# Kernel tuning notes

Measured on AMD Instinct MI355X. Metric: run time of the kernel, lower is better.

The kernel has to match this reference:

```python
import jax, jax.numpy as jnp
import numpy as np

TEMPERATURE = 1.0  # SpriteAssembler.compositing_temperature
EPS = 1e-6


def setup_inputs() -> dict:
    key = jax.random.key(0)
    k1, k2 = jax.random.split(key)
    B, H, W, N = 8, 256, 256, 64
    shapes = jax.random.uniform(k1, (B, H, W, N), dtype=jnp.float32)  # occupancy in [0,1]
    depths = jax.random.normal(k2, (B, N), dtype=jnp.float32)
    return {"shapes": shapes, "depths": depths}


def reference(shapes, depths):
    # custom_composite: depth-ordered log-space alpha compositing.
    # mask_i = s_i * prod_j (1 - s_j) ** tanh(relu((d_j - d_i)/T)), then normalize.
    d = depths / max(TEMPERATURE, 1e-6)                      # [B, N]
    s = jnp.clip(shapes, EPS, 1.0 - EPS)                     # [B, H, W, N]
    # occlusion weights: w[b, i, j] = tanh(relu(d_j - d_i))
    w = jnp.tanh(jax.nn.relu(d[:, None, :] - d[:, :, None]))  # [B, N, N]
    log1m = jnp.log1p(-s)                                    # log(1 - s), [B, H, W, N]
    # log_mask_i = log(s_i) + sum_j log(1 - s_j) * w[i, j]  (j == i term is 0 since w[i,i]=0)
    log_masks = jnp.log(s) + jnp.einsum('bhwj,bij->bhwi', log1m, w)
    unnormalized = jnp.exp(log_masks)                        # [B, H, W, N]
    masks = unnormalized / (jnp.sum(unnormalized, axis=-1, keepdims=True) + EPS)
    return masks
```

## Files before the change

kernel.cpp:

```cpp
#include <hip/hip_runtime.h>


typedef __attribute__((ext_vector_type(8))) _Float16 half8;
typedef __attribute__((ext_vector_type(4))) float floatx4;

#define EPSF 1e-6f

__device__ inline float fast_exp2(float x){ return __builtin_amdgcn_exp2f(x); }
__device__ inline float fast_log2(float x){ return __builtin_amdgcn_logf(x); }
__device__ inline float fast_rcp (float x){ return __builtin_amdgcn_rcpf(x); }

__global__ __launch_bounds__(256, 2) void sprite_mfma_kernel(
    const float* __restrict__ shapes,
    const float* __restrict__ depths,
    float* __restrict__ out)
{
    const int wave  = threadIdx.x >> 6;
    const int lane  = threadIdx.x & 63;
    const int batch = blockIdx.x >> 7;
    const int rblk  = blockIdx.x & 127;
    const int wid   = rblk * 4 + wave;

    __shared__ float dsh[64];
    if (threadIdx.x < 64) dsh[threadIdx.x] = depths[batch * 64 + threadIdx.x];
    __syncthreads();

    const int c = lane & 15;
    const int q = lane >> 4;

    half8 Aw[4][2];
    #pragma unroll
    for (int it = 0; it < 4; ++it) {
        float di = dsh[it * 16 + c];
        #pragma unroll
        for (int kt = 0; kt < 2; ++kt) {
            half8 h;
            #pragma unroll
            for (int jj = 0; jj < 8; ++jj) {
                int j = kt * 32 + q * 8 + jj;
                float x = fmaxf(dsh[j] - di, 0.0f);
                float e = fast_exp2(x * 2.885390082f);
                h[jj] = (_Float16)((e - 1.0f) * fast_rcp(e + 1.0f));
            }
            Aw[it][kt] = h;
        }
    }

    half8 idlo, idhi;
    #pragma unroll
    for (int jj = 0; jj < 8; ++jj) {
        idlo[jj] = (q * 8 + jj == c)      ? (_Float16)1.0f : (_Float16)0.0f;
        idhi[jj] = (q * 8 + jj == 16 + c) ? (_Float16)1.0f : (_Float16)0.0f;
    }

    const long pxbase = (long)batch * 65536 + (long)wid * 128;
    const float* sp = shapes + (pxbase + c) * 64;
    float* op = out + (pxbase + c) * 64;

    float4 pf0 = *(const float4*)(sp + q * 8);
    float4 pf1 = *(const float4*)(sp + q * 8 + 4);
    float4 pf2 = *(const float4*)(sp + q * 8 + 32);
    float4 pf3 = *(const float4*)(sp + q * 8 + 36);

    for (int tile = 0; tile < 8; ++tile) {
        float4 s0 = pf0, s1 = pf1, s2 = pf2, s3 = pf3;
        if (tile < 7) {
            const float* sn = sp + (tile + 1) * 16 * 64 + q * 8;
            pf0 = *(const float4*)(sn);
            pf1 = *(const float4*)(sn + 4);
            pf2 = *(const float4*)(sn + 32);
            pf3 = *(const float4*)(sn + 36);
        }

        float sv[16] = {s0.x, s0.y, s0.z, s0.w, s1.x, s1.y, s1.z, s1.w,
                        s2.x, s2.y, s2.z, s2.w, s3.x, s3.y, s3.z, s3.w};
        half8 B_lo, B_hi;
        half8 C_lo, C_hi;
        #pragma unroll
        for (int e = 0; e < 8; ++e) {
            float slo = fminf(fmaxf(sv[e],     EPSF), 1.0f - EPSF);
            float shi = fminf(fmaxf(sv[8 + e], EPSF), 1.0f - EPSF);
            B_lo[e] = (_Float16)fast_log2(1.0f - slo);
            B_hi[e] = (_Float16)fast_log2(1.0f - shi);
            C_lo[e] = (_Float16)fast_log2(slo);
            C_hi[e] = (_Float16)fast_log2(shi);
        }

        floatx4 acc[4];
        #pragma unroll
        for (int it = 0; it < 4; ++it) {
            floatx4 a = {0.f, 0.f, 0.f, 0.f};
            a = __builtin_amdgcn_mfma_f32_16x16x32_f16(Aw[it][0], B_lo, a, 0, 0, 0);
            a = __builtin_amdgcn_mfma_f32_16x16x32_f16(Aw[it][1], B_hi, a, 0, 0, 0);
            a = __builtin_amdgcn_mfma_f32_16x16x32_f16(
                    (it & 1) ? idhi : idlo, (it < 2) ? C_lo : C_hi, a, 0, 0, 0);
            acc[it] = a;
        }

        float u[4][4];
        float tot = 0.f;
        #pragma unroll
        for (int it = 0; it < 4; ++it) {
            #pragma unroll
            for (int r = 0; r < 4; ++r) {
                float v = fast_exp2(acc[it][r]);
                u[it][r] = v;
                tot += v;
            }
        }
        tot += __shfl_xor(tot, 16, 64);
        tot += __shfl_xor(tot, 32, 64);
        float inv = fast_rcp(tot + EPSF);

        float* orow = op + tile * 16 * 64;
        #pragma unroll
        for (int it = 0; it < 4; ++it) {
            float4 o = {u[it][0] * inv, u[it][1] * inv,
                        u[it][2] * inv, u[it][3] * inv};
            *(float4*)(orow + it * 16 + q * 4) = o;
        }
    }
}

extern "C" void kernel_launch(void* const* d_in, const int* in_sizes, int n_in,
                              void* d_out, int out_size, void* d_ws, size_t ws_size,
                              hipStream_t stream) {
    const float* shapes = (const float*)d_in[0];
    const float* depths = (const float*)d_in[1];
    float* out = (float*)d_out;
    sprite_mfma_kernel<<<1024, 256, 0, stream>>>(shapes, depths, out);
}
```

Baseline: 248.5 us.

## Stage input tiles through LDS with async global_load_lds triple buffering

Replaces the per-lane register prefetch of shape tiles with asynchronous global-to-LDS loads into a per-wave triple-buffered, XOR-swizzled staging area. Manual vmcnt waits track in-flight loads, which are interleaved with output stores, so more tiles can be in flight while compute proceeds. Occupancy hint is raised from 2 to 3 blocks per CU. The hand-counted vmcnt values and the LDS footprint are fragile, and the swizzled reads must still match the MFMA operand layout.

```diff
diff --git a/kernel.cpp b/kernel.cpp
--- a/kernel.cpp
+++ b/kernel.cpp
@@ -10,7 +10,10 @@
 __device__ inline float fast_log2(float x){ return __builtin_amdgcn_logf(x); }
 __device__ inline float fast_rcp (float x){ return __builtin_amdgcn_rcpf(x); }
 
-__global__ __launch_bounds__(256, 2) void sprite_mfma_kernel(
+#define WAITVM(N) asm volatile("s_waitcnt vmcnt(" #N ")" ::: "memory")
+#define VMFENCE() asm volatile("" ::: "memory")
+
+__global__ __launch_bounds__(256, 3) void sprite_mfma_kernel(
     const float* __restrict__ shapes,
     const float* __restrict__ depths,
     float* __restrict__ out)
@@ -22,11 +25,44 @@
     const int wid   = rblk * 4 + wave;
 
     __shared__ float dsh[64];
+    __shared__ __align__(16) char stage_lds[4][3][4096];
+
     if (threadIdx.x < 64) dsh[threadIdx.x] = depths[batch * 64 + threadIdx.x];
     __syncthreads();
 
     const int c = lane & 15;
     const int q = lane >> 4;
+
+    int gsw[4];
+    #pragma unroll
+    for (int k = 0; k < 4; ++k) {
+        int row = k * 4 + (lane >> 4);
+        int sw  = ((row & 7) << 5) ^ ((row & 8) << 1);
+        gsw[k]  = row * 256 + (((lane & 15) * 16) ^ sw);
+    }
+    const int rsw = ((c & 7) << 5) ^ ((c & 8) << 1);
+    const int a0 = c * 256 + (((q * 32)      ) ^ rsw);
+    const int a1 = c * 256 + (((q * 32) +  16) ^ rsw);
+    const int a2 = c * 256 + (((q * 32) + 128) ^ rsw);
+    const int a3 = c * 256 + (((q * 32) + 144) ^ rsw);
+
+    const long pxbase = (long)batch * 65536 + (long)wid * 128;
+    const char* gwave = (const char*)(shapes + pxbase * 64);
+    float* op = out + (pxbase + c) * 64;
+
+#define STAGE(T, SLOT) do {                                                   \
+    const char* _g = gwave + (T) * 4096;                                      \
+    char* _l = stage_lds[wave][(SLOT)];                                       \
+    _Pragma("unroll")                                                         \
+    for (int _k = 0; _k < 4; ++_k)                                            \
+        __builtin_amdgcn_global_load_lds(                                     \
+            (const __attribute__((address_space(1))) void*)(_g + gsw[_k]),    \
+            (__attribute__((address_space(3))) void*)(_l + _k * 1024),        \
+            16, 0, 0);                                                        \
+} while (0)
+
+    STAGE(0, 0);
+    STAGE(1, 1);
 
     half8 Aw[4][2];
     #pragma unroll
@@ -45,7 +81,6 @@
             Aw[it][kt] = h;
         }
     }
-
     half8 idlo, idhi;
     #pragma unroll
     for (int jj = 0; jj < 8; ++jj) {
@@ -53,25 +88,7 @@
         idhi[jj] = (q * 8 + jj == 16 + c) ? (_Float16)1.0f : (_Float16)0.0f;
     }
 
-    const long pxbase = (long)batch * 65536 + (long)wid * 128;
-    const float* sp = shapes + (pxbase + c) * 64;
-    float* op = out + (pxbase + c) * 64;
-
-    float4 pf0 = *(const float4*)(sp + q * 8);
-    float4 pf1 = *(const float4*)(sp + q * 8 + 4);
-    float4 pf2 = *(const float4*)(sp + q * 8 + 32);
-    float4 pf3 = *(const float4*)(sp + q * 8 + 36);
-
-    for (int tile = 0; tile < 8; ++tile) {
-        float4 s0 = pf0, s1 = pf1, s2 = pf2, s3 = pf3;
-        if (tile < 7) {
-            const float* sn = sp + (tile + 1) * 16 * 64 + q * 8;
-            pf0 = *(const float4*)(sn);
-            pf1 = *(const float4*)(sn + 4);
-            pf2 = *(const float4*)(sn + 32);
-            pf3 = *(const float4*)(sn + 36);
-        }
-
+    auto process = [&](float4 s0, float4 s1, float4 s2, float4 s3, int tile) {
         float sv[16] = {s0.x, s0.y, s0.z, s0.w, s1.x, s1.y, s1.z, s1.w,
                         s2.x, s2.y, s2.z, s2.w, s3.x, s3.y, s3.z, s3.w};
         half8 B_lo, B_hi;
@@ -115,11 +132,36 @@
         float* orow = op + tile * 16 * 64;
         #pragma unroll
         for (int it = 0; it < 4; ++it) {
-            float4 o = {u[it][0] * inv, u[it][1] * inv,
-                        u[it][2] * inv, u[it][3] * inv};
-            *(float4*)(orow + it * 16 + q * 4) = o;
+            floatx4 o = {u[it][0] * inv, u[it][1] * inv,
+                         u[it][2] * inv, u[it][3] * inv};
+            *(floatx4*)(orow + it * 16 + q * 4) = o;
         }
-    }
+    };
+
+#define TILE(T, SLOT, NW, DOSTAGE, NSLOT) do {                                \
+    WAITVM(NW);                                                               \
+    __builtin_amdgcn_sched_barrier(0);                                        \
+    const char* tb = stage_lds[wave][(SLOT)];                                 \
+    float4 v0 = *(const float4*)(tb + a0);                                    \
+    float4 v1 = *(const float4*)(tb + a1);                                    \
+    float4 v2 = *(const float4*)(tb + a2);                                    \
+    float4 v3 = *(const float4*)(tb + a3);                                    \
+    if (DOSTAGE) STAGE((T) + 2, NSLOT);                                       \
+    VMFENCE();                                                                \
+    process(v0, v1, v2, v3, (T));                                             \
+} while (0)
+
+    TILE(0, 0,  4, 1, 2);
+    TILE(1, 1,  8, 1, 0);
+    TILE(2, 2, 12, 1, 1);
+    TILE(3, 0, 12, 1, 2);
+    TILE(4, 1, 12, 1, 0);
+    TILE(5, 2, 12, 1, 1);
+    TILE(6, 0, 12, 0, 0);
+    TILE(7, 1,  8, 0, 0);
+
+#undef TILE
+#undef STAGE
 }
 
 extern "C" void kernel_launch(void* const* d_in, const int* in_sizes, int n_in,
```

New measurement: 234.9 us. 1.06x faster.
